# Kernel tuning notes

Hardware: AMD Instinct MI355X
Metric: run time of the kernel (lower is better)

Reference implementation:

```python
import jax, jax.numpy as jnp
import numpy as np

N = 100000      # nodes
E = 1600000     # edges
IN = 128        # in_channels
ED = 32         # edge_dim
H = 4           # heads
C = 32          # out_channels per head
NEG_SLOPE = 0.2


def setup_inputs() -> dict:
    key = jax.random.key(0)
    ks = jax.random.split(key, 10)
    s = 0.1  # glorot-ish scale
    return {
        "x": jax.random.normal(ks[0], (N, IN), dtype=jnp.float32),
        "edge_index": jax.random.randint(ks[1], (2, E), 0, N, dtype=jnp.int32),
        "edge_attr": jax.random.normal(ks[2], (E, ED), dtype=jnp.float32),
        "W": jax.random.normal(ks[3], (IN, H * C), dtype=jnp.float32) * s,
        "att_src": jax.random.normal(ks[4], (H, C), dtype=jnp.float32) * s,
        "att_dst": jax.random.normal(ks[5], (H, C), dtype=jnp.float32) * s,
        "W_edge": jax.random.normal(ks[6], (ED, H * C), dtype=jnp.float32) * s,
        "att_edge": jax.random.normal(ks[7], (H, C), dtype=jnp.float32) * s,
        "gat_bias": jnp.zeros((H * C,), dtype=jnp.float32),
        "bias": jnp.zeros((C,), dtype=jnp.float32),
    }


def reference(x, edge_index, edge_attr, W, att_src, att_dst, W_edge, att_edge, gat_bias, bias):
    # eval mode: no dropout. GATConv with edge_dim, concat=True, then mean over heads.
    src, dst = edge_index[0], edge_index[1]
    xh = (x @ W).reshape(N, H, C)                       # [N,H,C]
    a_src = jnp.einsum("nhc,hc->nh", xh, att_src)      # [N,H]
    a_dst = jnp.einsum("nhc,hc->nh", xh, att_dst)      # [N,H]
    eh = (edge_attr @ W_edge).reshape(E, H, C)          # [E,H,C]
    a_edge = jnp.einsum("ehc,hc->eh", eh, att_edge)    # [E,H]
    logits = a_src[src] + a_dst[dst] + a_edge           # [E,H]
    logits = jnp.where(logits >= 0, logits, NEG_SLOPE * logits)  # leaky_relu
    # segment softmax over edges grouped by destination node
    seg_max = jax.ops.segment_max(logits, dst, num_segments=N)  # [N,H]
    expv = jnp.exp(logits - seg_max[dst])
    denom = jax.ops.segment_sum(expv, dst, num_segments=N)      # [N,H]
    alpha = expv / denom[dst]                                    # [E,H]
    msg = xh[src] * alpha[:, :, None]                            # [E,H,C]
    out = jax.ops.segment_sum(msg, dst, num_segments=N)          # [N,H,C]
    out = out + gat_bias.reshape(1, H, C)                        # GATConv bias (concat)
    out = out.mean(axis=1)                                       # combine='mean' -> [N,C]
    out = out + bias
    return jax.nn.relu(out)
```

## Files before the change

### kernel.cpp

```cpp
#include <hip/hip_runtime.h>
#include <hip/hip_bf16.h>

typedef __hip_bfloat16 bf16;

#define N_NODES 100000
#define N_EDGES 1600000
#define IN_CH   128
#define ED_DIM  32
#define HEADS   4
#define C_OUT   32
#define HC      128
#define NEG_SLOPE 0.2f
#define SCAN_BLOCKS 98
#define BP_SLICES 8
#define BP_SLICE_N 12500
#define BP_CHUNKS 6250
#define PREP_BLOCKS 392
#define NG_BLOCKS 3125

__device__ __forceinline__ float bf_lo(unsigned u) { return __uint_as_float(u << 16); }
__device__ __forceinline__ float bf_hi(unsigned u) { return __uint_as_float(u & 0xffff0000u); }
__device__ __forceinline__ unsigned short f2bf_rne(float f) {
    unsigned u = __float_as_uint(f);
    return (unsigned short)((u + 0x7fffu + ((u >> 16) & 1u)) >> 16);
}
__device__ __forceinline__ unsigned pack_bf2(float a, float b) {
    return ((unsigned)f2bf_rne(b) << 16) | f2bf_rne(a);
}
__device__ __forceinline__ float load_any(const void* p, int i, int isf32) {
    return isf32 ? ((const float*)p)[i]
                 : __uint_as_float(((unsigned)((const unsigned short*)p)[i]) << 16);
}

__global__ void report_err(unsigned short* out, float code) {
    if (threadIdx.x < 16) out[threadIdx.x] = f2bf_rne(code);
}

__global__ __launch_bounds__(256) void prep_small(
    const void* __restrict__ x,
    const void* __restrict__ W, const void* __restrict__ att_src,
    const void* __restrict__ att_dst, const void* __restrict__ W_edge,
    const void* __restrict__ att_edge, const void* __restrict__ gat_bias,
    const void* __restrict__ bias,
    int* __restrict__ flag,
    unsigned short* __restrict__ Wc, float* __restrict__ att_src_f,
    float* __restrict__ att_dst_f, float* __restrict__ gat_bias_f,
    float* __restrict__ bias_f, float* __restrict__ Wa,
    int* __restrict__ count) {

    int t = threadIdx.x;
    int gi = blockIdx.x * 256 + t;
    if (gi < N_NODES) count[gi] = 0;
    if (blockIdx.x != 0) return;

    __shared__ int cnt;
    if (t == 0) cnt = 0;
    __syncthreads();
    unsigned xw = ((const unsigned*)x)[t];
    int ex = (xw >> 7) & 0xFF;
    if (ex >= 140) atomicAdd(&cnt, 1);
    __syncthreads();
    int isf32 = (cnt >= 32) ? 1 : 0;
    if (t == 0) *flag = isf32;

    for (int i = t; i < IN_CH * HC; i += 256)
        Wc[i] = f2bf_rne(load_any(W, i, isf32));
    if (t < 128) {
        att_src_f[t]  = load_any(att_src, t, isf32);
        att_dst_f[t]  = load_any(att_dst, t, isf32);
        gat_bias_f[t] = load_any(gat_bias, t, isf32);
    }
    if (t < 32) bias_f[t] = load_any(bias, t, isf32);
    if (t < 128) {
        int d = t & 31, h = t >> 5;
        float acc = 0.f;
        for (int c = 0; c < C_OUT; ++c)
            acc += load_any(W_edge, d * HC + h * C_OUT + c, isf32) *
                   load_any(att_edge, h * C_OUT + c, isf32);
        Wa[h * 32 + d] = acc;
    }
}

__global__ __launch_bounds__(256) void node_gemm(
    const int* __restrict__ flag, const void* __restrict__ x,
    const int* __restrict__ ei,
    const unsigned short* __restrict__ Wc,
    const float* __restrict__ att_src_f, const float* __restrict__ att_dst_f,
    unsigned short* __restrict__ xh,
    float* __restrict__ a_src, float* __restrict__ a_dst,
    int* __restrict__ count) {

    __shared__ unsigned short Wl[IN_CH * HC];
    __shared__ float xl[32 * IN_CH];

    int isf32 = *flag;
    int t = threadIdx.x;
    int node0 = blockIdx.x * 32;

    {
        const uint2* dst2 = (const uint2*)(ei + N_EDGES);
        uint2 d2 = dst2[blockIdx.x * 256 + t];
        atomicAdd(&count[d2.x], 1);
        atomicAdd(&count[d2.y], 1);
    }

    const uint4* Wg = (const uint4*)Wc;
    uint4* Wl4 = (uint4*)Wl;
#pragma unroll
    for (int k = 0; k < 8; ++k) Wl4[t + k * 256] = Wg[t + k * 256];

    if (isf32) {
        const float4* xg = (const float4*)((const float*)x + (size_t)node0 * IN_CH);
        float4* xl4 = (float4*)xl;
#pragma unroll
        for (int k = 0; k < 4; ++k) xl4[t + k * 256] = xg[t + k * 256];
    } else {
        const unsigned* xg = (const unsigned*)((const unsigned short*)x + (size_t)node0 * IN_CH);
#pragma unroll
        for (int k = 0; k < 8; ++k) {
            unsigned u = xg[t + k * 256];
            int f = 2 * (t + k * 256);
            xl[f]     = bf_lo(u);
            xl[f + 1] = bf_hi(u);
        }
    }
    __syncthreads();

    int q  = t & 31;
    int i0 = (t >> 5) * 4;
    int j4 = q * 4;
    float acc[16];
#pragma unroll
    for (int k = 0; k < 16; ++k) acc[k] = 0.f;

    const float* xr0 = xl + (i0 + 0) * IN_CH;
    const float* xr1 = xl + (i0 + 1) * IN_CH;
    const float* xr2 = xl + (i0 + 2) * IN_CH;
    const float* xr3 = xl + (i0 + 3) * IN_CH;

#pragma unroll 8
    for (int d = 0; d < IN_CH; ++d) {
        uint2 wb = *(const uint2*)(Wl + d * HC + j4);
        float w0 = bf_lo(wb.x), w1 = bf_hi(wb.x);
        float w2 = bf_lo(wb.y), w3 = bf_hi(wb.y);
        float x0 = xr0[d], x1 = xr1[d], x2 = xr2[d], x3 = xr3[d];
        acc[0]  += x0 * w0; acc[1]  += x0 * w1; acc[2]  += x0 * w2; acc[3]  += x0 * w3;
        acc[4]  += x1 * w0; acc[5]  += x1 * w1; acc[6]  += x1 * w2; acc[7]  += x1 * w3;
        acc[8]  += x2 * w0; acc[9]  += x2 * w1; acc[10] += x2 * w2; acc[11] += x2 * w3;
        acc[12] += x3 * w0; acc[13] += x3 * w1; acc[14] += x3 * w2; acc[15] += x3 * w3;
    }

    float4 sa = *(const float4*)(att_src_f + j4);
    float4 da = *(const float4*)(att_dst_f + j4);

#pragma unroll
    for (int k = 0; k < 4; ++k) {
        int node = node0 + i0 + k;
        float a0 = acc[4 * k], a1 = acc[4 * k + 1], a2 = acc[4 * k + 2], a3 = acc[4 * k + 3];
        *(uint2*)(xh + (size_t)node * HC + j4) =
            make_uint2(pack_bf2(a0, a1), pack_bf2(a2, a3));

        float ps = a0 * sa.x + a1 * sa.y + a2 * sa.z + a3 * sa.w;
        float pd = a0 * da.x + a1 * da.y + a2 * da.z + a3 * da.w;
        ps += __shfl_xor(ps, 1); ps += __shfl_xor(ps, 2); ps += __shfl_xor(ps, 4);
        pd += __shfl_xor(pd, 1); pd += __shfl_xor(pd, 2); pd += __shfl_xor(pd, 4);
        if ((q & 7) == 0) {
            int h = q >> 3;
            a_src[node * HEADS + h] = ps;
            a_dst[node * HEADS + h] = pd;
        }
    }
}

__global__ __launch_bounds__(256) void scan_a(const int* __restrict__ count,
                                              int* __restrict__ starts,
                                              int* __restrict__ blockSums) {
    __shared__ int sd[256];
    int t = threadIdx.x;
    int base = blockIdx.x * 1024 + t * 4;
    int c0 = (base + 0 < N_NODES) ? count[base + 0] : 0;
    int c1 = (base + 1 < N_NODES) ? count[base + 1] : 0;
    int c2 = (base + 2 < N_NODES) ? count[base + 2] : 0;
    int c3 = (base + 3 < N_NODES) ? count[base + 3] : 0;
    int s = c0 + c1 + c2 + c3;
    sd[t] = s;
    __syncthreads();
    for (int off = 1; off < 256; off <<= 1) {
        int v = (t >= off) ? sd[t - off] : 0;
        __syncthreads();
        sd[t] += v;
        __syncthreads();
    }
    int excl = sd[t] - s;
    if (base + 0 < N_NODES) starts[base + 0] = excl;
    if (base + 1 < N_NODES) starts[base + 1] = excl + c0;
    if (base + 2 < N_NODES) starts[base + 2] = excl + c0 + c1;
    if (base + 3 < N_NODES) starts[base + 3] = excl + c0 + c1 + c2;
    if (t == 255) blockSums[blockIdx.x] = sd[255];
}

__global__ __launch_bounds__(128) void scan_b(int* __restrict__ blockSums) {
    __shared__ int sd[128];
    int t = threadIdx.x;
    int v = (t < SCAN_BLOCKS) ? blockSums[t] : 0;
    sd[t] = v;
    __syncthreads();
    for (int off = 1; off < 128; off <<= 1) {
        int u = (t >= off) ? sd[t - off] : 0;
        __syncthreads();
        sd[t] += u;
        __syncthreads();
    }
    if (t < SCAN_BLOCKS) blockSums[t] = sd[t] - v;
}

__global__ __launch_bounds__(256) void scan_c(int* __restrict__ starts,
                                              int* __restrict__ cursor,
                                              const int* __restrict__ blockSums) {
    int off = blockSums[blockIdx.x];
    int base = blockIdx.x * 1024 + threadIdx.x * 4;
#pragma unroll
    for (int k = 0; k < 4; ++k) {
        int idx = base + k;
        if (idx < N_NODES) {
            int v = starts[idx] + off;
            starts[idx] = v;
            cursor[idx] = v;
        }
    }
    if (blockIdx.x == 0 && threadIdx.x == 0) starts[N_NODES] = N_EDGES;
}

__global__ __launch_bounds__(256) void edge_scatter(
    const int* __restrict__ flag,
    const int* __restrict__ ei, const void* __restrict__ edge_attr,
    const float* __restrict__ a_src, const float* __restrict__ a_dst,
    const float* __restrict__ Wa,
    int* __restrict__ cursor, uint4* __restrict__ perm4) {

    __shared__ float WaL[128];
    int t = threadIdx.x;
    if (t < 128) WaL[t] = Wa[t];
    __syncthreads();

    int slice = blockIdx.x & 7;
    int e = (blockIdx.x >> 3) * 256 + t;
    if (e >= N_EDGES) return;
    int dn = ei[N_EDGES + e];
    if (dn < slice * BP_SLICE_N || dn >= (slice + 1) * BP_SLICE_N) return;
    int s = ei[e];
    int isf32 = *flag;

    float ae0 = 0.f, ae1 = 0.f, ae2 = 0.f, ae3 = 0.f;
    if (isf32) {
        const float4* ea = (const float4*)((const float*)edge_attr + (size_t)e * ED_DIM);
#pragma unroll
        for (int k = 0; k < 8; ++k) {
            float4 v = ea[k];
            int d = 4 * k;
            ae0 += v.x * WaL[d] + v.y * WaL[d + 1] + v.z * WaL[d + 2] + v.w * WaL[d + 3];
            ae1 += v.x * WaL[32 + d] + v.y * WaL[33 + d] + v.z * WaL[34 + d] + v.w * WaL[35 + d];
            ae2 += v.x * WaL[64 + d] + v.y * WaL[65 + d] + v.z * WaL[66 + d] + v.w * WaL[67 + d];
            ae3 += v.x * WaL[96 + d] + v.y * WaL[97 + d] + v.z * WaL[98 + d] + v.w * WaL[99 + d];
        }
    } else {
        const uint4* ea = (const uint4*)((const unsigned short*)edge_attr + (size_t)e * ED_DIM);
#pragma unroll
        for (int k = 0; k < 4; ++k) {
            uint4 v = ea[k];
            float g0 = bf_lo(v.x), g1 = bf_hi(v.x), g2 = bf_lo(v.y), g3 = bf_hi(v.y);
            float g4 = bf_lo(v.z), g5 = bf_hi(v.z), g6 = bf_lo(v.w), g7 = bf_hi(v.w);
            int d = 8 * k;
            ae0 += g0*WaL[d] + g1*WaL[d+1] + g2*WaL[d+2] + g3*WaL[d+3]
                 + g4*WaL[d+4] + g5*WaL[d+5] + g6*WaL[d+6] + g7*WaL[d+7];
            ae1 += g0*WaL[32+d] + g1*WaL[33+d] + g2*WaL[34+d] + g3*WaL[35+d]
                 + g4*WaL[36+d] + g5*WaL[37+d] + g6*WaL[38+d] + g7*WaL[39+d];
            ae2 += g0*WaL[64+d] + g1*WaL[65+d] + g2*WaL[66+d] + g3*WaL[67+d]
                 + g4*WaL[68+d] + g5*WaL[69+d] + g6*WaL[70+d] + g7*WaL[71+d];
            ae3 += g0*WaL[96+d] + g1*WaL[97+d] + g2*WaL[98+d] + g3*WaL[99+d]
                 + g4*WaL[100+d] + g5*WaL[101+d] + g6*WaL[102+d] + g7*WaL[103+d];
        }
    }

    float4 as = *(const float4*)(a_src + (size_t)s * 4);
    float4 ad = *(const float4*)(a_dst + (size_t)dn * 4);
    float l0 = as.x + ad.x + ae0;
    float l1 = as.y + ad.y + ae1;
    float l2 = as.z + ad.z + ae2;
    float l3 = as.w + ad.w + ae3;
    l0 = (l0 >= 0.f) ? l0 : NEG_SLOPE * l0;
    l1 = (l1 >= 0.f) ? l1 : NEG_SLOPE * l1;
    l2 = (l2 >= 0.f) ? l2 : NEG_SLOPE * l2;
    l3 = (l3 >= 0.f) ? l3 : NEG_SLOPE * l3;
    float w0 = __expf(l0), w1 = __expf(l1), w2 = __expf(l2), w3 = __expf(l3);

    int pos = atomicAdd(&cursor[dn], 1);
    perm4[pos] = make_uint4((unsigned)s, pack_bf2(w0, w1), pack_bf2(w2, w3), 0u);
}

__global__ __launch_bounds__(256) void gather(
    const int* __restrict__ flag,
    const int* __restrict__ starts, const uint4* __restrict__ perm4,
    const unsigned short* __restrict__ xh,
    const float* __restrict__ gat_bias_f, const float* __restrict__ bias_f,
    void* __restrict__ out) {

    __shared__ uint4 sR[4][64];

    int t = threadIdx.x;
    int w = t >> 6, lane = t & 63;
    int quarter = lane >> 4;
    int l = lane & 15;
    int h = l >> 2;
    int n = blockIdx.x * 4 + w;
    if (n >= N_NODES) return;
    int isf32 = *flag;

    int st = starts[n], en = starts[n + 1];
    float f0 = 0.f, f1 = 0.f, f2 = 0.f, f3 = 0.f;
    float f4 = 0.f, f5 = 0.f, f6 = 0.f, f7 = 0.f, wsum = 0.f;

    for (int base = st; base < en; base += 64) {
        int cnt = en - base;
        if (cnt > 64) cnt = 64;
        __builtin_amdgcn_wave_barrier();
        if (lane < cnt) sR[w][lane] = perm4[base + lane];
        __builtin_amdgcn_wave_barrier();
#pragma unroll 4
        for (int jj = 0; jj < cnt; jj += 4) {
            int j = jj + quarter;
            int valid = (j < cnt);
            int jc = valid ? j : jj;
            uint4 r = sR[w][jc];
            int s = (int)r.x;
            unsigned hw = (h & 2) ? r.z : r.y;
            float wt = (h & 1) ? bf_hi(hw) : bf_lo(hw);
            wt = valid ? wt : 0.f;
            uint4 xv = *(const uint4*)(xh + ((size_t)s << 7) + 8 * l);
            f0 += wt * bf_lo(xv.x);
            f1 += wt * bf_hi(xv.x);
            f2 += wt * bf_lo(xv.y);
            f3 += wt * bf_hi(xv.y);
            f4 += wt * bf_lo(xv.z);
            f5 += wt * bf_hi(xv.z);
            f6 += wt * bf_lo(xv.w);
            f7 += wt * bf_hi(xv.w);
            wsum += wt;
        }
    }

    f0 += __shfl_xor(f0, 16); f0 += __shfl_xor(f0, 32);
    f1 += __shfl_xor(f1, 16); f1 += __shfl_xor(f1, 32);
    f2 += __shfl_xor(f2, 16); f2 += __shfl_xor(f2, 32);
    f3 += __shfl_xor(f3, 16); f3 += __shfl_xor(f3, 32);
    f4 += __shfl_xor(f4, 16); f4 += __shfl_xor(f4, 32);
    f5 += __shfl_xor(f5, 16); f5 += __shfl_xor(f5, 32);
    f6 += __shfl_xor(f6, 16); f6 += __shfl_xor(f6, 32);
    f7 += __shfl_xor(f7, 16); f7 += __shfl_xor(f7, 32);
    wsum += __shfl_xor(wsum, 16); wsum += __shfl_xor(wsum, 32);

    float inv = (wsum > 0.f) ? 1.f / wsum : 0.f;
    int cg = 8 * l;
    float v0 = f0 * inv + gat_bias_f[cg];
    float v1 = f1 * inv + gat_bias_f[cg + 1];
    float v2 = f2 * inv + gat_bias_f[cg + 2];
    float v3 = f3 * inv + gat_bias_f[cg + 3];
    float v4 = f4 * inv + gat_bias_f[cg + 4];
    float v5 = f5 * inv + gat_bias_f[cg + 5];
    float v6 = f6 * inv + gat_bias_f[cg + 6];
    float v7 = f7 * inv + gat_bias_f[cg + 7];
    v0 += __shfl_xor(v0, 4); v0 += __shfl_xor(v0, 8);
    v1 += __shfl_xor(v1, 4); v1 += __shfl_xor(v1, 8);
    v2 += __shfl_xor(v2, 4); v2 += __shfl_xor(v2, 8);
    v3 += __shfl_xor(v3, 4); v3 += __shfl_xor(v3, 8);
    v4 += __shfl_xor(v4, 4); v4 += __shfl_xor(v4, 8);
    v5 += __shfl_xor(v5, 4); v5 += __shfl_xor(v5, 8);
    v6 += __shfl_xor(v6, 4); v6 += __shfl_xor(v6, 8);
    v7 += __shfl_xor(v7, 4); v7 += __shfl_xor(v7, 8);

    if (lane < 4) {
        int c = 8 * lane;
        float o0 = fmaxf(v0 * 0.25f + bias_f[c],     0.f);
        float o1 = fmaxf(v1 * 0.25f + bias_f[c + 1], 0.f);
        float o2 = fmaxf(v2 * 0.25f + bias_f[c + 2], 0.f);
        float o3 = fmaxf(v3 * 0.25f + bias_f[c + 3], 0.f);
        float o4 = fmaxf(v4 * 0.25f + bias_f[c + 4], 0.f);
        float o5 = fmaxf(v5 * 0.25f + bias_f[c + 5], 0.f);
        float o6 = fmaxf(v6 * 0.25f + bias_f[c + 6], 0.f);
        float o7 = fmaxf(v7 * 0.25f + bias_f[c + 7], 0.f);
        if (isf32) {
            float* op = (float*)out + (size_t)n * C_OUT + c;
            *(float4*)(op)     = make_float4(o0, o1, o2, o3);
            *(float4*)(op + 4) = make_float4(o4, o5, o6, o7);
        } else {
            unsigned p0 = ((unsigned)f2bf_rne(o1) << 16) | f2bf_rne(o0);
            unsigned p1 = ((unsigned)f2bf_rne(o3) << 16) | f2bf_rne(o2);
            unsigned p2 = ((unsigned)f2bf_rne(o5) << 16) | f2bf_rne(o4);
            unsigned p3 = ((unsigned)f2bf_rne(o7) << 16) | f2bf_rne(o6);
            *(uint4*)((unsigned short*)out + (size_t)n * C_OUT + c) =
                make_uint4(p0, p1, p2, p3);
        }
    }
}

extern "C" void kernel_launch(void* const* d_in, const int* in_sizes, int n_in,
                              void* d_out, int out_size, void* d_ws, size_t ws_size,
                              hipStream_t stream) {
    const void* x         = d_in[0];
    const int*  ei        = (const int*)d_in[1];
    const void* edge_attr = d_in[2];
    const void* W         = d_in[3];
    const void* att_src   = d_in[4];
    const void* att_dst   = d_in[5];
    const void* W_edge    = d_in[6];
    const void* att_edge  = d_in[7];
    const void* gat_bias  = d_in[8];
    const void* bias      = d_in[9];

    char* ws = (char*)d_ws;
    size_t off = 0;
    auto align256 = [](size_t v) { return (v + 255) & ~(size_t)255; };

    unsigned short* xh = (unsigned short*)(ws + off);
    off = align256(off + (size_t)N_NODES * HC * sizeof(unsigned short));
    float* a_src_w = (float*)(ws + off);
    off = align256(off + (size_t)N_NODES * HEADS * sizeof(float));
    float* a_dst_w = (float*)(ws + off);
    off = align256(off + (size_t)N_NODES * HEADS * sizeof(float));
    int* count = (int*)(ws + off);
    off = align256(off + (size_t)N_NODES * sizeof(int));
    int* starts = (int*)(ws + off);
    off = align256(off + (size_t)(N_NODES + 1) * sizeof(int));
    int* cursor = (int*)(ws + off);
    off = align256(off + (size_t)N_NODES * sizeof(int));
    int* blockSums = (int*)(ws + off);
    off = align256(off + (size_t)SCAN_BLOCKS * sizeof(int));
    uint4* perm4 = (uint4*)(ws + off);
    off = align256(off + (size_t)N_EDGES * sizeof(uint4));
    float* Wa = (float*)(ws + off);
    off = align256(off + 128 * sizeof(float));
    unsigned short* Wc = (unsigned short*)(ws + off);
    off = align256(off + (size_t)IN_CH * HC * sizeof(unsigned short));
    float* att_src_f = (float*)(ws + off);
    off = align256(off + 128 * sizeof(float));
    float* att_dst_f = (float*)(ws + off);
    off = align256(off + 128 * sizeof(float));
    float* gat_bias_f = (float*)(ws + off);
    off = align256(off + 128 * sizeof(float));
    float* bias_f = (float*)(ws + off);
    off = align256(off + 32 * sizeof(float));
    int* dflag = (int*)(ws + off);
    off = align256(off + sizeof(int));
    size_t need = off;

    if (ws_size < need) {
        report_err<<<1, 64, 0, stream>>>((unsigned short*)d_out, 1500.0f);
        return;
    }

    (void)hipGetLastError();

    prep_small<<<PREP_BLOCKS, 256, 0, stream>>>(x, W, att_src, att_dst,
                                                W_edge, att_edge, gat_bias, bias,
                                                dflag, Wc, att_src_f, att_dst_f,
                                                gat_bias_f, bias_f, Wa, count);
    node_gemm<<<NG_BLOCKS, 256, 0, stream>>>(dflag, x, ei, Wc, att_src_f,
                                             att_dst_f, xh, a_src_w, a_dst_w,
                                             count);
    scan_a<<<SCAN_BLOCKS, 256, 0, stream>>>(count, starts, blockSums);
    scan_b<<<1, 128, 0, stream>>>(blockSums);
    scan_c<<<SCAN_BLOCKS, 256, 0, stream>>>(starts, cursor, blockSums);
    edge_scatter<<<BP_SLICES * BP_CHUNKS, 256, 0, stream>>>(dflag, ei, edge_attr,
                                                            a_src_w, a_dst_w, Wa,
                                                            cursor, perm4);
    gather<<<N_NODES / 4, 256, 0, stream>>>(dflag, starts, perm4,
                                            xh, gat_bias_f, bias_f, d_out);

    hipError_t e = hipGetLastError();
    if (e != hipSuccess) {
        report_err<<<1, 64, 0, stream>>>((unsigned short*)d_out,
                                         1000.0f + (float)(int)e);
    }
}
```

Measured before the change: 650.3 us.

## Split edge weight computation from slice-filtered scatter into separate kernels

Edge logit and exp computation moves out of the sliced scatter kernel into its own dense per-edge kernel, which writes packed bf16 weights to a new workspace buffer. The scatter kernel then only reads dst/src indices (two edges per thread) and the precomputed weights, and does the atomic placement. Before, each edge's edge_attr was read once and its weights computed once in whichever slice matched, but warps diverged. Now the edge_attr pass runs fully coalesced, at the cost of an extra 12.8MB write and read of the weights and one more kernel launch.

```diff
diff --git a/kernel.cpp b/kernel.cpp
--- a/kernel.cpp
+++ b/kernel.cpp
@@ -14,7 +14,7 @@
 #define SCAN_BLOCKS 98
 #define BP_SLICES 8
 #define BP_SLICE_N 12500
-#define BP_CHUNKS 6250
+#define BP_CHUNKS2 3125
 #define PREP_BLOCKS 392
 #define NG_BLOCKS 3125
 
@@ -170,6 +170,70 @@
             a_dst[node * HEADS + h] = pd;
         }
     }
+}
+
+__global__ __launch_bounds__(256) void edge_w(
+    const int* __restrict__ flag,
+    const int* __restrict__ ei, const void* __restrict__ edge_attr,
+    const float* __restrict__ a_src, const float* __restrict__ a_dst,
+    const float* __restrict__ Wa,
+    uint2* __restrict__ w4b) {
+
+    __shared__ float WaL[128];
+    int t = threadIdx.x;
+    if (t < 128) WaL[t] = Wa[t];
+    __syncthreads();
+
+    int isf32 = *flag;
+    int e = blockIdx.x * 256 + t;
+    if (e >= N_EDGES) return;
+    int s  = ei[e];
+    int dn = ei[N_EDGES + e];
+
+    float ae0 = 0.f, ae1 = 0.f, ae2 = 0.f, ae3 = 0.f;
+    if (isf32) {
+        const float4* ea = (const float4*)((const float*)edge_attr + (size_t)e * ED_DIM);
+#pragma unroll
+        for (int k = 0; k < 8; ++k) {
+            float4 v = ea[k];
+            int d = 4 * k;
+            ae0 += v.x * WaL[d] + v.y * WaL[d + 1] + v.z * WaL[d + 2] + v.w * WaL[d + 3];
+            ae1 += v.x * WaL[32 + d] + v.y * WaL[33 + d] + v.z * WaL[34 + d] + v.w * WaL[35 + d];
+            ae2 += v.x * WaL[64 + d] + v.y * WaL[65 + d] + v.z * WaL[66 + d] + v.w * WaL[67 + d];
+            ae3 += v.x * WaL[96 + d] + v.y * WaL[97 + d] + v.z * WaL[98 + d] + v.w * WaL[99 + d];
+        }
+    } else {
+        const uint4* ea = (const uint4*)((const unsigned short*)edge_attr + (size_t)e * ED_DIM);
+#pragma unroll
+        for (int k = 0; k < 4; ++k) {
+            uint4 v = ea[k];
+            float g0 = bf_lo(v.x), g1 = bf_hi(v.x), g2 = bf_lo(v.y), g3 = bf_hi(v.y);
+            float g4 = bf_lo(v.z), g5 = bf_hi(v.z), g6 = bf_lo(v.w), g7 = bf_hi(v.w);
+            int d = 8 * k;
+            ae0 += g0*WaL[d] + g1*WaL[d+1] + g2*WaL[d+2] + g3*WaL[d+3]
+                 + g4*WaL[d+4] + g5*WaL[d+5] + g6*WaL[d+6] + g7*WaL[d+7];
+            ae1 += g0*WaL[32+d] + g1*WaL[33+d] + g2*WaL[34+d] + g3*WaL[35+d]
+                 + g4*WaL[36+d] + g5*WaL[37+d] + g6*WaL[38+d] + g7*WaL[39+d];
+            ae2 += g0*WaL[64+d] + g1*WaL[65+d] + g2*WaL[66+d] + g3*WaL[67+d]
+                 + g4*WaL[68+d] + g5*WaL[69+d] + g6*WaL[70+d] + g7*WaL[71+d];
+            ae3 += g0*WaL[96+d] + g1*WaL[97+d] + g2*WaL[98+d] + g3*WaL[99+d]
+                 + g4*WaL[100+d] + g5*WaL[101+d] + g6*WaL[102+d] + g7*WaL[103+d];
+        }
+    }
+
+    float4 as = *(const float4*)(a_src + (size_t)s * 4);
+    float4 ad = *(const float4*)(a_dst + (size_t)dn * 4);
+    float l0 = as.x + ad.x + ae0;
+    float l1 = as.y + ad.y + ae1;
+    float l2 = as.z + ad.z + ae2;
+    float l3 = as.w + ad.w + ae3;
+    l0 = (l0 >= 0.f) ? l0 : NEG_SLOPE * l0;
+    l1 = (l1 >= 0.f) ? l1 : NEG_SLOPE * l1;
+    l2 = (l2 >= 0.f) ? l2 : NEG_SLOPE * l2;
+    l3 = (l3 >= 0.f) ? l3 : NEG_SLOPE * l3;
+    float w0 = __expf(l0), w1 = __expf(l1), w2 = __expf(l2), w3 = __expf(l3);
+
+    w4b[e] = make_uint2(pack_bf2(w0, w1), pack_bf2(w2, w3));
 }
 
 __global__ __launch_bounds__(256) void scan_a(const int* __restrict__ count,
@@ -231,71 +295,30 @@
     if (blockIdx.x == 0 && threadIdx.x == 0) starts[N_NODES] = N_EDGES;
 }
 
-__global__ __launch_bounds__(256) void edge_scatter(
-    const int* __restrict__ flag,
-    const int* __restrict__ ei, const void* __restrict__ edge_attr,
-    const float* __restrict__ a_src, const float* __restrict__ a_dst,
-    const float* __restrict__ Wa,
+__global__ __launch_bounds__(256) void build_perm(
+    const int* __restrict__ ei, const uint2* __restrict__ w4b,
     int* __restrict__ cursor, uint4* __restrict__ perm4) {
-
-    __shared__ float WaL[128];
-    int t = threadIdx.x;
-    if (t < 128) WaL[t] = Wa[t];
-    __syncthreads();
-
     int slice = blockIdx.x & 7;
-    int e = (blockIdx.x >> 3) * 256 + t;
-    if (e >= N_EDGES) return;
-    int dn = ei[N_EDGES + e];
-    if (dn < slice * BP_SLICE_N || dn >= (slice + 1) * BP_SLICE_N) return;
-    int s = ei[e];
-    int isf32 = *flag;
-
-    float ae0 = 0.f, ae1 = 0.f, ae2 = 0.f, ae3 = 0.f;
-    if (isf32) {
-        const float4* ea = (const float4*)((const float*)edge_attr + (size_t)e * ED_DIM);
-#pragma unroll
-        for (int k = 0; k < 8; ++k) {
-            float4 v = ea[k];
-            int d = 4 * k;
-            ae0 += v.x * WaL[d] + v.y * WaL[d + 1] + v.z * WaL[d + 2] + v.w * WaL[d + 3];
-            ae1 += v.x * WaL[32 + d] + v.y * WaL[33 + d] + v.z * WaL[34 + d] + v.w * WaL[35 + d];
-            ae2 += v.x * WaL[64 + d] + v.y * WaL[65 + d] + v.z * WaL[66 + d] + v.w * WaL[67 + d];
-            ae3 += v.x * WaL[96 + d] + v.y * WaL[97 + d] + v.z * WaL[98 + d] + v.w * WaL[99 + d];
-        }
-    } else {
-        const uint4* ea = (const uint4*)((const unsigned short*)edge_attr + (size_t)e * ED_DIM);
-#pragma unroll
-        for (int k = 0; k < 4; ++k) {
-            uint4 v = ea[k];
-            float g0 = bf_lo(v.x), g1 = bf_hi(v.x), g2 = bf_lo(v.y), g3 = bf_hi(v.y);
-            float g4 = bf_lo(v.z), g5 = bf_hi(v.z), g6 = bf_lo(v.w), g7 = bf_hi(v.w);
-            int d = 8 * k;
-            ae0 += g0*WaL[d] + g1*WaL[d+1] + g2*WaL[d+2] + g3*WaL[d+3]
-                 + g4*WaL[d+4] + g5*WaL[d+5] + g6*WaL[d+6] + g7*WaL[d+7];
-            ae1 += g0*WaL[32+d] + g1*WaL[33+d] + g2*WaL[34+d] + g3*WaL[35+d]
-                 + g4*WaL[36+d] + g5*WaL[37+d] + g6*WaL[38+d] + g7*WaL[39+d];
-            ae2 += g0*WaL[64+d] + g1*WaL[65+d] + g2*WaL[66+d] + g3*WaL[67+d]
-                 + g4*WaL[68+d] + g5*WaL[69+d] + g6*WaL[70+d] + g7*WaL[71+d];
-            ae3 += g0*WaL[96+d] + g1*WaL[97+d] + g2*WaL[98+d] + g3*WaL[99+d]
-                 + g4*WaL[100+d] + g5*WaL[101+d] + g6*WaL[102+d] + g7*WaL[103+d];
-        }
-    }
-
-    float4 as = *(const float4*)(a_src + (size_t)s * 4);
-    float4 ad = *(const float4*)(a_dst + (size_t)dn * 4);
-    float l0 = as.x + ad.x + ae0;
-    float l1 = as.y + ad.y + ae1;
-    float l2 = as.z + ad.z + ae2;
-    float l3 = as.w + ad.w + ae3;
-    l0 = (l0 >= 0.f) ? l0 : NEG_SLOPE * l0;
-    l1 = (l1 >= 0.f) ? l1 : NEG_SLOPE * l1;
-    l2 = (l2 >= 0.f) ? l2 : NEG_SLOPE * l2;
-    l3 = (l3 >= 0.f) ? l3 : NEG_SLOPE * l3;
-    float w0 = __expf(l0), w1 = __expf(l1), w2 = __expf(l2), w3 = __expf(l3);
-
-    int pos = atomicAdd(&cursor[dn], 1);
-    perm4[pos] = make_uint4((unsigned)s, pack_bf2(w0, w1), pack_bf2(w2, w3), 0u);
+    int lo = slice * BP_SLICE_N, hi = lo + BP_SLICE_N;
+    int p = (blockIdx.x >> 3) * 256 + threadIdx.x;
+    int e0 = 2 * p;
+    const uint2* dst2 = (const uint2*)(ei + N_EDGES);
+    const uint2* src2 = (const uint2*)ei;
+    uint2 d2 = dst2[p];
+    int m0 = ((int)d2.x >= lo) & ((int)d2.x < hi);
+    int m1 = ((int)d2.y >= lo) & ((int)d2.y < hi);
+    if (!(m0 | m1)) return;
+    uint2 s2 = src2[p];
+    if (m0) {
+        uint2 wv = w4b[e0];
+        int pos = atomicAdd(&cursor[d2.x], 1);
+        perm4[pos] = make_uint4(s2.x, wv.x, wv.y, 0u);
+    }
+    if (m1) {
+        uint2 wv = w4b[e0 + 1];
+        int pos = atomicAdd(&cursor[d2.y], 1);
+        perm4[pos] = make_uint4(s2.y, wv.x, wv.y, 0u);
+    }
 }
 
 __global__ __launch_bounds__(256) void gather(
@@ -435,6 +458,8 @@
     off = align256(off + (size_t)N_NODES * sizeof(int));
     int* blockSums = (int*)(ws + off);
     off = align256(off + (size_t)SCAN_BLOCKS * sizeof(int));
+    uint2* w4b = (uint2*)(ws + off);
+    off = align256(off + (size_t)N_EDGES * sizeof(uint2));
     uint4* perm4 = (uint4*)(ws + off);
     off = align256(off + (size_t)N_EDGES * sizeof(uint4));
     float* Wa = (float*)(ws + off);
@@ -467,12 +492,12 @@
     node_gemm<<<NG_BLOCKS, 256, 0, stream>>>(dflag, x, ei, Wc, att_src_f,
                                              att_dst_f, xh, a_src_w, a_dst_w,
                                              count);
+    edge_w<<<(N_EDGES + 255) / 256, 256, 0, stream>>>(dflag, ei, edge_attr,
+                                                      a_src_w, a_dst_w, Wa, w4b);
     scan_a<<<SCAN_BLOCKS, 256, 0, stream>>>(count, starts, blockSums);
     scan_b<<<1, 128, 0, stream>>>(blockSums);
     scan_c<<<SCAN_BLOCKS, 256, 0, stream>>>(starts, cursor, blockSums);
-    edge_scatter<<<BP_SLICES * BP_CHUNKS, 256, 0, stream>>>(dflag, ei, edge_attr,
-                                                            a_src_w, a_dst_w, Wa,
-                                                            cursor, perm4);
+    build_perm<<<BP_SLICES * BP_CHUNKS2, 256, 0, stream>>>(ei, w4b, cursor, perm4);
     gather<<<N_NODES / 4, 256, 0, stream>>>(dflag, starts, perm4,
                                             xh, gat_bias_f, bias_f, d_out);
 
```

Result: faster. 577.7 us (-11.2%).
